# Performance work log

Measured on AMD Instinct MI355X. Metric: run time of the kernel, lower is better.

The kernel has to match this reference:

```python
import jax, jax.numpy as jnp
import numpy as np

OUT, IN, R = 4096, 4096, 64
B, S = 4, 4096


def setup_inputs() -> dict:
    key = jax.random.key(0)
    ks = jax.random.split(key, 12)
    return {
        "x": jax.random.normal(ks[0], (B, S, IN), dtype=jnp.float32),
        "W": jax.random.normal(ks[1], (OUT, IN), dtype=jnp.float32) * 0.02,
        "bias": jax.random.normal(ks[2], (OUT,), dtype=jnp.float32) * 0.02,
        "U_top": jax.random.normal(ks[3], (OUT, R), dtype=jnp.float32) / np.sqrt(OUT),
        "S_top": jax.random.uniform(ks[4], (R,), dtype=jnp.float32),
        "Vh_top": jax.random.normal(ks[5], (R, IN), dtype=jnp.float32) / np.sqrt(IN),
        "U_tail": jax.random.normal(ks[6], (OUT, R), dtype=jnp.float32) / np.sqrt(OUT),
        "S_tail": jax.random.uniform(ks[7], (R,), dtype=jnp.float32),
        "Vh_tail": jax.random.normal(ks[8], (R, IN), dtype=jnp.float32) / np.sqrt(IN),
        "alpha": jax.random.normal(ks[9], (R,), dtype=jnp.float32) * 0.01,
        "beta": jax.random.normal(ks[10], (R,), dtype=jnp.float32) * 0.01,
        "R": jax.random.normal(ks[11], (R, R), dtype=jnp.float32) * 0.01,
    }


def reference(x, W, bias, U_top, S_top, Vh_top, U_tail, S_tail, Vh_tail, alpha, beta, R):
    # SALT top: gated singular-value correction, relu(S*alpha + beta)
    sigma_top = jax.nn.relu(S_top * alpha + beta)                    # [r]
    W_top_delta = (U_top * sigma_top[None, :]) @ Vh_top              # [out, in]
    # EDoRA tail: B R A with B = U_tail diag(S_tail), A = Vh_tail
    Bm = U_tail * S_tail[None, :]                                    # [out, r]
    delta_tail = Bm @ (R @ Vh_tail)                                  # [out, in]
    W_tilde = W + W_top_delta + delta_tail
    # F.linear: x @ W_tilde.T + bias
    return jnp.einsum('bsi,oi->bso', x, W_tilde) + bias
```

## Files before the change

### kernel.cpp

```cpp
#include <hip/hip_runtime.h>
#include <hip/hip_bf16.h>

#define OUT_DIM 4096
#define IN_DIM  4096
#define RANK    64
#define M_DIM   16384

typedef short  s16x8 __attribute__((ext_vector_type(8)));
typedef __bf16 b16x8 __attribute__((ext_vector_type(8)));
typedef float  f32x4 __attribute__((ext_vector_type(4)));

template <typename T>
__device__ static inline auto mfma_sel(T a, T b, f32x4 c, int)
    -> decltype(__builtin_amdgcn_mfma_f32_16x16x32_bf16(a, b, c, 0, 0, 0)) {
  return __builtin_amdgcn_mfma_f32_16x16x32_bf16(a, b, c, 0, 0, 0);
}
template <typename T>
__device__ static inline f32x4 mfma_sel(T a, T b, f32x4 c, long) {
  return __builtin_amdgcn_mfma_f32_16x16x32_bf16(
      __builtin_bit_cast(b16x8, a), __builtin_bit_cast(b16x8, b), c, 0, 0, 0);
}
__device__ static inline f32x4 mfma_bf16(s16x8 a, s16x8 b, f32x4 c) {
  return mfma_sel(a, b, c, 0);
}

__device__ static inline unsigned short f2bf(float f) {
  unsigned int u = __float_as_uint(f);
  u += 0x7fffu + ((u >> 16) & 1u);
  return (unsigned short)(u >> 16);
}

__device__ static inline void gload16(const unsigned short* g, unsigned short* l) {
  __builtin_amdgcn_global_load_lds(
      (const __attribute__((address_space(1))) void*)g,
      (__attribute__((address_space(3))) void*)l, 16, 0, 0);
}

__global__ void prep_kernel(const float* __restrict__ U_top, const float* __restrict__ S_top,
                            const float* __restrict__ alpha, const float* __restrict__ beta,
                            const float* __restrict__ U_tail, const float* __restrict__ S_tail,
                            float* __restrict__ A1, float* __restrict__ A2) {
  int idx = blockIdx.x * 256 + threadIdx.x;
  int r = idx & (RANK - 1);
  float sig = S_top[r] * alpha[r] + beta[r];
  sig = sig > 0.f ? sig : 0.f;
  A1[idx] = U_top[idx] * sig;
  A2[idx] = U_tail[idx] * S_tail[r];
}

__global__ void rv_kernel(const float* __restrict__ Rm, const float* __restrict__ Vh_tail,
                          float* __restrict__ RV) {
  const int i  = blockIdx.x * 256 + threadIdx.x;
  const int r0 = blockIdx.y * 8;
  float acc[8] = {};
  for (int q = 0; q < RANK; ++q) {
    float v = Vh_tail[(size_t)q * IN_DIM + i];
#pragma unroll
    for (int rr = 0; rr < 8; ++rr)
      acc[rr] = fmaf(Rm[(r0 + rr) * RANK + q], v, acc[rr]);
  }
#pragma unroll
  for (int rr = 0; rr < 8; ++rr) RV[(size_t)(r0 + rr) * IN_DIM + i] = acc[rr];
}

__global__ void cvt_kernel(const float* __restrict__ x, unsigned short* __restrict__ xb) {
  const long long n8 = (long long)M_DIM * IN_DIM / 8;
  long long idx = (long long)blockIdx.x * blockDim.x + threadIdx.x;
  const long long stride = (long long)gridDim.x * blockDim.x;
  for (; idx < n8; idx += stride) {
    const f32x4* p = (const f32x4*)(x + idx * 8);
    f32x4 v0 = p[0], v1 = p[1];
    s16x8 o;
    o[0] = (short)f2bf(v0[0]); o[1] = (short)f2bf(v0[1]);
    o[2] = (short)f2bf(v0[2]); o[3] = (short)f2bf(v0[3]);
    o[4] = (short)f2bf(v1[0]); o[5] = (short)f2bf(v1[1]);
    o[6] = (short)f2bf(v1[2]); o[7] = (short)f2bf(v1[3]);
    *(s16x8*)(xb + idx * 8) = o;
  }
}

#define WT_O 16
__global__ void wtilde_kernel(const float* __restrict__ W,  const float* __restrict__ A1,
                              const float* __restrict__ A2, const float* __restrict__ Vh_top,
                              const float* __restrict__ RV, unsigned short* __restrict__ Wb) {
  const int i  = blockIdx.x * 256 + threadIdx.x;
  const int o0 = blockIdx.y * WT_O;
  float acc[WT_O];
#pragma unroll
  for (int o = 0; o < WT_O; ++o) acc[o] = W[(size_t)(o0 + o) * IN_DIM + i];
#pragma unroll 4
  for (int r = 0; r < RANK; ++r) {
    float vt = Vh_top[(size_t)r * IN_DIM + i];
    float rv = RV[(size_t)r * IN_DIM + i];
#pragma unroll
    for (int o = 0; o < WT_O; ++o) {
      acc[o] = fmaf(A1[(o0 + o) * RANK + r], vt, acc[o]);
      acc[o] = fmaf(A2[(o0 + o) * RANK + r], rv, acc[o]);
    }
  }
#pragma unroll
  for (int o = 0; o < WT_O; ++o)
    Wb[(size_t)(o0 + o) * IN_DIM + i] = f2bf(acc[o]);
}

#define BM 256
#define BN 256
#define BK 64
#define NT (IN_DIM / BK)

__global__ __launch_bounds__(512, 2) void gemm_kernel(
    const unsigned short* __restrict__ A,
    const unsigned short* __restrict__ Bw,
    const float* __restrict__ bias,
    float* __restrict__ C) {
  __shared__ unsigned short lds[2][2][BM * BK];

  const int tid = threadIdx.x;
  const int l   = tid & 63;
  const int wid = tid >> 6;
  const int wr  = wid >> 2;
  const int wc  = wid & 3;

  const int bid = blockIdx.x;
  const int swz = (bid & 7) * 128 + (bid >> 3);
  const int nt_ = swz >> 6;
  const int mt_ = swz & 63;
  const long long tileM = (long long)mt_ * BM;
  const long long tileN = (long long)nt_ * BN;

  const int rbase = tid >> 3;
  const int c8    = (((tid & 7) ^ (rbase & 7)) << 3);
  const unsigned short* gA = A  + (tileM + rbase) * (long long)IN_DIM + c8;
  const unsigned short* gB = Bw + (tileN + rbase) * (long long)IN_DIM + c8;

  const int kgrp = l >> 4;
  const int x7   = l & 7;
  const int sc0  = (((0 * 4 + kgrp) ^ x7) << 3);
  const int sc1  = (((1 * 4 + kgrp) ^ x7) << 3);
  const int rba  = (wr * 128 + (l & 15)) * BK;
  const int rbb  = (wc * 64  + (l & 15)) * BK;

  f32x4 acc[8][4] = {};

  {
    unsigned short* la = &lds[0][0][tid * 8];
    unsigned short* lb = &lds[0][1][tid * 8];
#pragma unroll
    for (int j = 0; j < 4; ++j) {
      gload16(gA + (long long)j * 64 * IN_DIM, la + j * 4096);
      gload16(gB + (long long)j * 64 * IN_DIM, lb + j * 4096);
    }
    asm volatile("s_waitcnt vmcnt(0)" ::: "memory");
    asm volatile("s_barrier" ::: "memory");
  }

  int buf = 0;
  for (int t = 0; t < NT; ++t) {
    const long long ktn = (long long)(t + 1) * BK;
    const bool more = (t + 1 < NT);
    const unsigned short* lA = lds[buf][0];
    const unsigned short* lB = lds[buf][1];
    unsigned short* la1 = &lds[buf ^ 1][0][tid * 8];
    unsigned short* lb1 = &lds[buf ^ 1][1][tid * 8];

    s16x8 bfr[4][2];
#pragma unroll
    for (int q = 0; q < 4; ++q) {
      if (q == 0) {
#pragma unroll
        for (int n = 0; n < 4; ++n) {
          bfr[n][0] = *(const s16x8*)&lB[rbb + n * 16 * BK + sc0];
          bfr[n][1] = *(const s16x8*)&lB[rbb + n * 16 * BK + sc1];
        }
      }
      s16x8 afr[2][2];
#pragma unroll
      for (int m2 = 0; m2 < 2; ++m2) {
        afr[m2][0] = *(const s16x8*)&lA[rba + (q * 32 + m2 * 16) * BK + sc0];
        afr[m2][1] = *(const s16x8*)&lA[rba + (q * 32 + m2 * 16) * BK + sc1];
      }

      if (more) {
        if (q == 0) {
          gload16(gA + ktn, la1);
          gload16(gA + ktn + 2LL * 64 * IN_DIM, la1 + 2 * 4096);
        } else if (q == 1) {
          gload16(gA + ktn + 1LL * 64 * IN_DIM, la1 + 1 * 4096);
          gload16(gA + ktn + 3LL * 64 * IN_DIM, la1 + 3 * 4096);
        } else if (q == 2) {
          gload16(gB + ktn, lb1);
          gload16(gB + ktn + 1LL * 64 * IN_DIM, lb1 + 4096);
        } else {
          gload16(gB + ktn + 2LL * 64 * IN_DIM, lb1 + 2 * 4096);
          gload16(gB + ktn + 3LL * 64 * IN_DIM, lb1 + 3 * 4096);
        }
      }

      asm volatile("s_barrier" ::: "memory");

      __builtin_amdgcn_s_setprio(1);
#pragma unroll
      for (int m2 = 0; m2 < 2; ++m2)
#pragma unroll
        for (int n = 0; n < 4; ++n)
#pragma unroll
          for (int kk = 0; kk < 2; ++kk)
            acc[q * 2 + m2][n] = mfma_bf16(afr[m2][kk], bfr[n][kk], acc[q * 2 + m2][n]);
      __builtin_amdgcn_s_setprio(0);

      if (q == 3 && more) {
        asm volatile("s_waitcnt vmcnt(0)" ::: "memory");
      }
      asm volatile("s_barrier" ::: "memory");
    }
    buf ^= 1;
  }

  float bv[4];
#pragma unroll
  for (int n = 0; n < 4; ++n) bv[n] = bias[tileN + wc * 64 + n * 16 + (l & 15)];
#pragma unroll
  for (int m = 0; m < 8; ++m) {
    const long long rbase_c = tileM + wr * 128 + m * 16 + (l >> 4) * 4;
#pragma unroll
    for (int r = 0; r < 4; ++r) {
      float* crow = C + (size_t)(rbase_c + r) * OUT_DIM + tileN + wc * 64 + (l & 15);
#pragma unroll
      for (int n = 0; n < 4; ++n) crow[n * 16] = acc[m][n][r] + bv[n];
    }
  }
}

extern "C" void kernel_launch(void* const* d_in, const int* in_sizes, int n_in,
                              void* d_out, int out_size, void* d_ws, size_t ws_size,
                              hipStream_t stream) {
  const float* x       = (const float*)d_in[0];
  const float* W       = (const float*)d_in[1];
  const float* bias    = (const float*)d_in[2];
  const float* U_top   = (const float*)d_in[3];
  const float* S_top   = (const float*)d_in[4];
  const float* Vh_top  = (const float*)d_in[5];
  const float* U_tail  = (const float*)d_in[6];
  const float* S_tail  = (const float*)d_in[7];
  const float* Vh_tail = (const float*)d_in[8];
  const float* alpha   = (const float*)d_in[9];
  const float* beta    = (const float*)d_in[10];
  const float* Rm      = (const float*)d_in[11];

  char* ws = (char*)d_ws;
  unsigned short* xb = (unsigned short*)ws;
  unsigned short* Wb = (unsigned short*)(ws + (size_t)134217728);
  float* A1 = (float*)(ws + (size_t)134217728 + 33554432);
  float* A2 = A1 + (size_t)OUT_DIM * RANK;
  float* RV = A2 + (size_t)OUT_DIM * RANK;

  prep_kernel<<<(OUT_DIM * RANK) / 256, 256, 0, stream>>>(U_top, S_top, alpha, beta,
                                                          U_tail, S_tail, A1, A2);
  rv_kernel<<<dim3(IN_DIM / 256, RANK / 8), 256, 0, stream>>>(Rm, Vh_tail, RV);
  cvt_kernel<<<2048, 256, 0, stream>>>(x, xb);
  wtilde_kernel<<<dim3(IN_DIM / 256, OUT_DIM / WT_O), 256, 0, stream>>>(W, A1, A2,
                                                                        Vh_top, RV, Wb);
  gemm_kernel<<<(M_DIM / BM) * (OUT_DIM / BN), 512, 0, stream>>>(xb, Wb, bias,
                                                                 (float*)d_out);
}
```

Measured before the change: 761.1 us.

## Switch GEMM to 4-stage LDS ring with BK=32 and deeper prefetch

Replaces the double-buffered BK=64 main loop with a four-slot LDS ring of BK=32 tiles, keeping three tiles of global loads in flight and waiting with vmcnt(8) instead of draining to zero each iteration. The goal is to hide global-load latency better and cut the barriers per K-step from eight to one. The LDS swizzle is reworked for 32-wide rows. In exchange there are twice as many iterations, and each one now has a single barrier right after the LDS reads. This raises the risk of a write-after-read hazard on the slot being refilled, and of LDS bank conflicts with the new swizzle.

```diff
diff --git a/kernel.cpp b/kernel.cpp
--- a/kernel.cpp
+++ b/kernel.cpp
@@ -103,17 +103,17 @@
     Wb[(size_t)(o0 + o) * IN_DIM + i] = f2bf(acc[o]);
 }
 
-#define BM 256
-#define BN 256
-#define BK 64
-#define NT (IN_DIM / BK)
+#define BM  256
+#define BN  256
+#define BK2 32
+#define NT2 (IN_DIM / BK2)
 
 __global__ __launch_bounds__(512, 2) void gemm_kernel(
     const unsigned short* __restrict__ A,
     const unsigned short* __restrict__ Bw,
     const float* __restrict__ bias,
     float* __restrict__ C) {
-  __shared__ unsigned short lds[2][2][BM * BK];
+  __shared__ unsigned short lds[4][2][BM * BK2];
 
   const int tid = threadIdx.x;
   const int l   = tid & 63;
@@ -128,93 +128,67 @@
   const long long tileM = (long long)mt_ * BM;
   const long long tileN = (long long)nt_ * BN;
 
-  const int rbase = tid >> 3;
-  const int c8    = (((tid & 7) ^ (rbase & 7)) << 3);
-  const unsigned short* gA = A  + (tileM + rbase) * (long long)IN_DIM + c8;
-  const unsigned short* gB = Bw + (tileN + rbase) * (long long)IN_DIM + c8;
-
-  const int kgrp = l >> 4;
-  const int x7   = l & 7;
-  const int sc0  = (((0 * 4 + kgrp) ^ x7) << 3);
-  const int sc1  = (((1 * 4 + kgrp) ^ x7) << 3);
-  const int rba  = (wr * 128 + (l & 15)) * BK;
-  const int rbb  = (wc * 64  + (l & 15)) * BK;
+  const int srow = tid >> 2;
+  const int sc_g = ((tid & 3) ^ ((srow & 7) >> 1)) * 8;
+  const unsigned short* gA = A  + (tileM + srow) * (long long)IN_DIM + sc_g;
+  const unsigned short* gB = Bw + (tileN + srow) * (long long)IN_DIM + sc_g;
+
+  const int sc   = (((l >> 4) ^ ((l & 7) >> 1)) << 3);
+  const int rbaA = (wr * 128 + (l & 15)) * BK2;
+  const int rbaB = (wc * 64  + (l & 15)) * BK2;
 
   f32x4 acc[8][4] = {};
 
-  {
-    unsigned short* la = &lds[0][0][tid * 8];
-    unsigned short* lb = &lds[0][1][tid * 8];
-#pragma unroll
-    for (int j = 0; j < 4; ++j) {
-      gload16(gA + (long long)j * 64 * IN_DIM, la + j * 4096);
-      gload16(gB + (long long)j * 64 * IN_DIM, lb + j * 4096);
+#pragma unroll
+  for (int tt = 0; tt < 3; ++tt) {
+    unsigned short* dA = &lds[tt][0][tid * 8];
+    unsigned short* dB = &lds[tt][1][tid * 8];
+    gload16(gA + tt * BK2, dA);
+    gload16(gA + tt * BK2 + 128LL * IN_DIM, dA + 4096);
+    gload16(gB + tt * BK2, dB);
+    gload16(gB + tt * BK2 + 128LL * IN_DIM, dB + 4096);
+  }
+  asm volatile("s_waitcnt vmcnt(8)" ::: "memory");
+  asm volatile("s_barrier" ::: "memory");
+
+  auto tile_body = [&](int T, bool issue) {
+    const unsigned short* lA = &lds[T & 3][0][0];
+    const unsigned short* lB = &lds[T & 3][1][0];
+    s16x8 af[8], bf[4];
+#pragma unroll
+    for (int m = 0; m < 8; ++m) af[m] = *(const s16x8*)&lA[rbaA + m * 512 + sc];
+#pragma unroll
+    for (int n = 0; n < 4; ++n) bf[n] = *(const s16x8*)&lB[rbaB + n * 512 + sc];
+    if (issue) {
+      const long long ko = (long long)(T + 3) * BK2;
+      unsigned short* dA = &lds[(T + 3) & 3][0][tid * 8];
+      unsigned short* dB = &lds[(T + 3) & 3][1][tid * 8];
+      gload16(gA + ko, dA);
+      gload16(gA + ko + 128LL * IN_DIM, dA + 4096);
+      gload16(gB + ko, dB);
+      gload16(gB + ko + 128LL * IN_DIM, dB + 4096);
     }
-    asm volatile("s_waitcnt vmcnt(0)" ::: "memory");
+    __builtin_amdgcn_s_setprio(1);
+#pragma unroll
+    for (int m = 0; m < 8; ++m)
+#pragma unroll
+      for (int n = 0; n < 4; ++n)
+        acc[m][n] = mfma_bf16(af[m], bf[n], acc[m][n]);
+    __builtin_amdgcn_s_setprio(0);
+  };
+
+  for (int t = 0; t < NT2 - 3; ++t) {
+    tile_body(t, true);
+    asm volatile("s_waitcnt vmcnt(8)" ::: "memory");
     asm volatile("s_barrier" ::: "memory");
   }
-
-  int buf = 0;
-  for (int t = 0; t < NT; ++t) {
-    const long long ktn = (long long)(t + 1) * BK;
-    const bool more = (t + 1 < NT);
-    const unsigned short* lA = lds[buf][0];
-    const unsigned short* lB = lds[buf][1];
-    unsigned short* la1 = &lds[buf ^ 1][0][tid * 8];
-    unsigned short* lb1 = &lds[buf ^ 1][1][tid * 8];
-
-    s16x8 bfr[4][2];
-#pragma unroll
-    for (int q = 0; q < 4; ++q) {
-      if (q == 0) {
-#pragma unroll
-        for (int n = 0; n < 4; ++n) {
-          bfr[n][0] = *(const s16x8*)&lB[rbb + n * 16 * BK + sc0];
-          bfr[n][1] = *(const s16x8*)&lB[rbb + n * 16 * BK + sc1];
-        }
-      }
-      s16x8 afr[2][2];
-#pragma unroll
-      for (int m2 = 0; m2 < 2; ++m2) {
-        afr[m2][0] = *(const s16x8*)&lA[rba + (q * 32 + m2 * 16) * BK + sc0];
-        afr[m2][1] = *(const s16x8*)&lA[rba + (q * 32 + m2 * 16) * BK + sc1];
-      }
-
-      if (more) {
-        if (q == 0) {
-          gload16(gA + ktn, la1);
-          gload16(gA + ktn + 2LL * 64 * IN_DIM, la1 + 2 * 4096);
-        } else if (q == 1) {
-          gload16(gA + ktn + 1LL * 64 * IN_DIM, la1 + 1 * 4096);
-          gload16(gA + ktn + 3LL * 64 * IN_DIM, la1 + 3 * 4096);
-        } else if (q == 2) {
-          gload16(gB + ktn, lb1);
-          gload16(gB + ktn + 1LL * 64 * IN_DIM, lb1 + 4096);
-        } else {
-          gload16(gB + ktn + 2LL * 64 * IN_DIM, lb1 + 2 * 4096);
-          gload16(gB + ktn + 3LL * 64 * IN_DIM, lb1 + 3 * 4096);
-        }
-      }
-
-      asm volatile("s_barrier" ::: "memory");
-
-      __builtin_amdgcn_s_setprio(1);
-#pragma unroll
-      for (int m2 = 0; m2 < 2; ++m2)
-#pragma unroll
-        for (int n = 0; n < 4; ++n)
-#pragma unroll
-          for (int kk = 0; kk < 2; ++kk)
-            acc[q * 2 + m2][n] = mfma_bf16(afr[m2][kk], bfr[n][kk], acc[q * 2 + m2][n]);
-      __builtin_amdgcn_s_setprio(0);
-
-      if (q == 3 && more) {
-        asm volatile("s_waitcnt vmcnt(0)" ::: "memory");
-      }
-      asm volatile("s_barrier" ::: "memory");
-    }
-    buf ^= 1;
-  }
+  tile_body(125, false);
+  asm volatile("s_waitcnt vmcnt(4)" ::: "memory");
+  asm volatile("s_barrier" ::: "memory");
+  tile_body(126, false);
+  asm volatile("s_waitcnt vmcnt(0)" ::: "memory");
+  asm volatile("s_barrier" ::: "memory");
+  tile_body(127, false);
 
   float bv[4];
 #pragma unroll
```

Result: no change. 756.9 us (-0.5%).

## Fuse prep kernels into one launch and relax GEMM load waits

Applied to the files above, without the earlier changes.

Drops the separate scale kernel by folding S_tail into the R@Vh_tail product and applying the sigma gating inline. The x bf16 conversion and the W_tilde build now run as one combined grid, which removes launches and lets the two phases overlap. In the GEMM main loop, B tiles are now loaded before A tiles. The full vmcnt(0) drain is replaced by partial waits, so the second half of the A tile can still be in flight while the first half is consumed. This relies on careful vmcnt accounting across iterations, which is easy to get wrong.

```diff
diff --git a/kernel.cpp b/kernel.cpp
--- a/kernel.cpp
+++ b/kernel.cpp
@@ -36,20 +36,8 @@
       (__attribute__((address_space(3))) void*)l, 16, 0, 0);
 }
 
-__global__ void prep_kernel(const float* __restrict__ U_top, const float* __restrict__ S_top,
-                            const float* __restrict__ alpha, const float* __restrict__ beta,
-                            const float* __restrict__ U_tail, const float* __restrict__ S_tail,
-                            float* __restrict__ A1, float* __restrict__ A2) {
-  int idx = blockIdx.x * 256 + threadIdx.x;
-  int r = idx & (RANK - 1);
-  float sig = S_top[r] * alpha[r] + beta[r];
-  sig = sig > 0.f ? sig : 0.f;
-  A1[idx] = U_top[idx] * sig;
-  A2[idx] = U_tail[idx] * S_tail[r];
-}
-
-__global__ void rv_kernel(const float* __restrict__ Rm, const float* __restrict__ Vh_tail,
-                          float* __restrict__ RV) {
+__global__ void rv2_kernel(const float* __restrict__ Rm, const float* __restrict__ Vh_tail,
+                           const float* __restrict__ S_tail, float* __restrict__ RV2) {
   const int i  = blockIdx.x * 256 + threadIdx.x;
   const int r0 = blockIdx.y * 8;
   float acc[8] = {};
@@ -60,47 +48,56 @@
       acc[rr] = fmaf(Rm[(r0 + rr) * RANK + q], v, acc[rr]);
   }
 #pragma unroll
-  for (int rr = 0; rr < 8; ++rr) RV[(size_t)(r0 + rr) * IN_DIM + i] = acc[rr];
-}
-
-__global__ void cvt_kernel(const float* __restrict__ x, unsigned short* __restrict__ xb) {
-  const long long n8 = (long long)M_DIM * IN_DIM / 8;
-  long long idx = (long long)blockIdx.x * blockDim.x + threadIdx.x;
-  const long long stride = (long long)gridDim.x * blockDim.x;
-  for (; idx < n8; idx += stride) {
-    const f32x4* p = (const f32x4*)(x + idx * 8);
-    f32x4 v0 = p[0], v1 = p[1];
-    s16x8 o;
-    o[0] = (short)f2bf(v0[0]); o[1] = (short)f2bf(v0[1]);
-    o[2] = (short)f2bf(v0[2]); o[3] = (short)f2bf(v0[3]);
-    o[4] = (short)f2bf(v1[0]); o[5] = (short)f2bf(v1[1]);
-    o[6] = (short)f2bf(v1[2]); o[7] = (short)f2bf(v1[3]);
-    *(s16x8*)(xb + idx * 8) = o;
-  }
-}
-
+  for (int rr = 0; rr < 8; ++rr)
+    RV2[(size_t)(r0 + rr) * IN_DIM + i] = acc[rr] * S_tail[r0 + rr];
+}
+
+#define CVT_BLOCKS 2048
 #define WT_O 16
-__global__ void wtilde_kernel(const float* __restrict__ W,  const float* __restrict__ A1,
-                              const float* __restrict__ A2, const float* __restrict__ Vh_top,
-                              const float* __restrict__ RV, unsigned short* __restrict__ Wb) {
-  const int i  = blockIdx.x * 256 + threadIdx.x;
-  const int o0 = blockIdx.y * WT_O;
-  float acc[WT_O];
-#pragma unroll
-  for (int o = 0; o < WT_O; ++o) acc[o] = W[(size_t)(o0 + o) * IN_DIM + i];
+#define WT_BLOCKS ((IN_DIM / 256) * (OUT_DIM / WT_O))
+__global__ void prep_fused_kernel(const float* __restrict__ x, unsigned short* __restrict__ xb,
+                                  const float* __restrict__ W,      const float* __restrict__ U_top,
+                                  const float* __restrict__ S_top,  const float* __restrict__ alpha,
+                                  const float* __restrict__ beta,   const float* __restrict__ U_tail,
+                                  const float* __restrict__ Vh_top, const float* __restrict__ RV2,
+                                  unsigned short* __restrict__ Wb) {
+  const int tid = threadIdx.x;
+  if (blockIdx.x < CVT_BLOCKS) {
+    const long long n8 = (long long)M_DIM * IN_DIM / 8;
+    long long idx = (long long)blockIdx.x * 256 + tid;
+    const long long stride = (long long)CVT_BLOCKS * 256;
+    for (; idx < n8; idx += stride) {
+      const f32x4* p = (const f32x4*)(x + idx * 8);
+      f32x4 v0 = p[0], v1 = p[1];
+      s16x8 o;
+      o[0] = (short)f2bf(v0[0]); o[1] = (short)f2bf(v0[1]);
+      o[2] = (short)f2bf(v0[2]); o[3] = (short)f2bf(v0[3]);
+      o[4] = (short)f2bf(v1[0]); o[5] = (short)f2bf(v1[1]);
+      o[6] = (short)f2bf(v1[2]); o[7] = (short)f2bf(v1[3]);
+      *(s16x8*)(xb + idx * 8) = o;
+    }
+  } else {
+    const int rem = blockIdx.x - CVT_BLOCKS;
+    const int i   = (rem & 15) * 256 + tid;
+    const int o0  = (rem >> 4) * WT_O;
+    float acc[WT_O];
+#pragma unroll
+    for (int o = 0; o < WT_O; ++o) acc[o] = W[(size_t)(o0 + o) * IN_DIM + i];
 #pragma unroll 4
-  for (int r = 0; r < RANK; ++r) {
-    float vt = Vh_top[(size_t)r * IN_DIM + i];
-    float rv = RV[(size_t)r * IN_DIM + i];
-#pragma unroll
-    for (int o = 0; o < WT_O; ++o) {
-      acc[o] = fmaf(A1[(o0 + o) * RANK + r], vt, acc[o]);
-      acc[o] = fmaf(A2[(o0 + o) * RANK + r], rv, acc[o]);
-    }
-  }
-#pragma unroll
-  for (int o = 0; o < WT_O; ++o)
-    Wb[(size_t)(o0 + o) * IN_DIM + i] = f2bf(acc[o]);
+    for (int r = 0; r < RANK; ++r) {
+      float sig = fmaxf(fmaf(S_top[r], alpha[r], beta[r]), 0.f);
+      float vt  = Vh_top[(size_t)r * IN_DIM + i] * sig;
+      float rv  = RV2[(size_t)r * IN_DIM + i];
+#pragma unroll
+      for (int o = 0; o < WT_O; ++o) {
+        acc[o] = fmaf(U_top[(o0 + o) * RANK + r],  vt, acc[o]);
+        acc[o] = fmaf(U_tail[(o0 + o) * RANK + r], rv, acc[o]);
+      }
+    }
+#pragma unroll
+    for (int o = 0; o < WT_O; ++o)
+      Wb[(size_t)(o0 + o) * IN_DIM + i] = f2bf(acc[o]);
+  }
 }
 
 #define BM 256
@@ -147,8 +144,8 @@
     unsigned short* lb = &lds[0][1][tid * 8];
 #pragma unroll
     for (int j = 0; j < 4; ++j) {
+      gload16(gB + (long long)j * 64 * IN_DIM, lb + j * 4096);
       gload16(gA + (long long)j * 64 * IN_DIM, la + j * 4096);
-      gload16(gB + (long long)j * 64 * IN_DIM, lb + j * 4096);
     }
     asm volatile("s_waitcnt vmcnt(0)" ::: "memory");
     asm volatile("s_barrier" ::: "memory");
@@ -182,17 +179,17 @@
 
       if (more) {
         if (q == 0) {
+          gload16(gB + ktn, lb1);
+          gload16(gB + ktn + 1LL * 64 * IN_DIM, lb1 + 4096);
+        } else if (q == 1) {
+          gload16(gB + ktn + 2LL * 64 * IN_DIM, lb1 + 2 * 4096);
+          gload16(gB + ktn + 3LL * 64 * IN_DIM, lb1 + 3 * 4096);
+        } else if (q == 2) {
           gload16(gA + ktn, la1);
           gload16(gA + ktn + 2LL * 64 * IN_DIM, la1 + 2 * 4096);
-        } else if (q == 1) {
+        } else {
           gload16(gA + ktn + 1LL * 64 * IN_DIM, la1 + 1 * 4096);
           gload16(gA + ktn + 3LL * 64 * IN_DIM, la1 + 3 * 4096);
-        } else if (q == 2) {
-          gload16(gB + ktn, lb1);
-          gload16(gB + ktn + 1LL * 64 * IN_DIM, lb1 + 4096);
-        } else {
-          gload16(gB + ktn + 2LL * 64 * IN_DIM, lb1 + 2 * 4096);
-          gload16(gB + ktn + 3LL * 64 * IN_DIM, lb1 + 3 * 4096);
         }
       }
 
@@ -208,8 +205,12 @@
             acc[q * 2 + m2][n] = mfma_bf16(afr[m2][kk], bfr[n][kk], acc[q * 2 + m2][n]);
       __builtin_amdgcn_s_setprio(0);
 
+      if (q == 1) {
+        if (more) asm volatile("s_waitcnt vmcnt(4)" ::: "memory");
+        else      asm volatile("s_waitcnt vmcnt(0)" ::: "memory");
+      }
       if (q == 3 && more) {
-        asm volatile("s_waitcnt vmcnt(0)" ::: "memory");
+        asm volatile("s_waitcnt vmcnt(2)" ::: "memory");
       }
       asm volatile("s_barrier" ::: "memory");
     }
@@ -248,18 +249,13 @@
   const float* Rm      = (const float*)d_in[11];
 
   char* ws = (char*)d_ws;
-  unsigned short* xb = (unsigned short*)ws;
-  unsigned short* Wb = (unsigned short*)(ws + (size_t)134217728);
-  float* A1 = (float*)(ws + (size_t)134217728 + 33554432);
-  float* A2 = A1 + (size_t)OUT_DIM * RANK;
-  float* RV = A2 + (size_t)OUT_DIM * RANK;
-
-  prep_kernel<<<(OUT_DIM * RANK) / 256, 256, 0, stream>>>(U_top, S_top, alpha, beta,
-                                                          U_tail, S_tail, A1, A2);
-  rv_kernel<<<dim3(IN_DIM / 256, RANK / 8), 256, 0, stream>>>(Rm, Vh_tail, RV);
-  cvt_kernel<<<2048, 256, 0, stream>>>(x, xb);
-  wtilde_kernel<<<dim3(IN_DIM / 256, OUT_DIM / WT_O), 256, 0, stream>>>(W, A1, A2,
-                                                                        Vh_top, RV, Wb);
+  unsigned short* xb  = (unsigned short*)ws;
+  unsigned short* Wb  = (unsigned short*)(ws + (size_t)134217728);
+  float*          RV2 = (float*)(ws + (size_t)134217728 + 33554432);
+
+  rv2_kernel<<<dim3(IN_DIM / 256, RANK / 8), 256, 0, stream>>>(Rm, Vh_tail, S_tail, RV2);
+  prep_fused_kernel<<<CVT_BLOCKS + WT_BLOCKS, 256, 0, stream>>>(
+      x, xb, W, U_top, S_top, alpha, beta, U_tail, Vh_top, RV2, Wb);
   gemm_kernel<<<(M_DIM / BM) * (OUT_DIM / BN), 512, 0, stream>>>(xb, Wb, bias,
                                                                  (float*)d_out);
 }
```

Result: faster. 702.8 us (-7.7%).
